# Performance work log

Hardware: AMD Instinct MI355X
Metric: run time of the kernel (lower is better)

## Reference

```python
import jax, jax.numpy as jnp
import numpy as np

NUM_HEADS = 14
NUM_KV_HEADS = 2
HEAD_DIM = 64
HIDDEN = 896
ROPE_THETA = 1000000.0
NEG_INF = -1e9


def _rope_tables(seq_len, dtype=jnp.float32):
    inv_freq = 1.0 / (ROPE_THETA ** (jnp.arange(0, HEAD_DIM, 2, dtype=jnp.float32) / HEAD_DIM))
    t = jnp.arange(seq_len, dtype=jnp.float32)
    freqs = t[:, None] * inv_freq[None, :]          # [S, hd/2]
    emb = jnp.concatenate((freqs, freqs), axis=-1)  # [S, hd]
    return jnp.cos(emb).astype(dtype), jnp.sin(emb).astype(dtype)


def _rotate_half(x):
    x1, x2 = x[..., : x.shape[-1] // 2], x[..., x.shape[-1] // 2 :]
    return jnp.concatenate((-x2, x1), axis=-1)


def setup_inputs() -> dict:
    key = jax.random.key(0)
    ks = jax.random.split(key, 6)
    B, S = 2, 2048
    hidden_states = jax.random.normal(ks[0], (B, S, HIDDEN), dtype=jnp.float32)
    # additive causal mask [1, 1, S, S]
    causal = jnp.tril(jnp.ones((S, S), dtype=bool))
    attention_mask = jnp.where(causal, 0.0, NEG_INF).astype(jnp.float32)[None, None]
    sd = 1.0 / np.sqrt(HIDDEN)
    Wq = jax.random.normal(ks[1], (HIDDEN, NUM_HEADS * HEAD_DIM), dtype=jnp.float32) * sd
    bq = jnp.zeros((NUM_HEADS * HEAD_DIM,), dtype=jnp.float32)
    Wk = jax.random.normal(ks[2], (HIDDEN, NUM_KV_HEADS * HEAD_DIM), dtype=jnp.float32) * sd
    bk = jnp.zeros((NUM_KV_HEADS * HEAD_DIM,), dtype=jnp.float32)
    Wv = jax.random.normal(ks[3], (HIDDEN, NUM_KV_HEADS * HEAD_DIM), dtype=jnp.float32) * sd
    bv = jnp.zeros((NUM_KV_HEADS * HEAD_DIM,), dtype=jnp.float32)
    Wo = jax.random.normal(ks[4], (NUM_HEADS * HEAD_DIM, HIDDEN), dtype=jnp.float32) * sd
    return {
        'hidden_states': hidden_states, 'attention_mask': attention_mask,
        'Wq': Wq, 'bq': bq, 'Wk': Wk, 'bk': bk, 'Wv': Wv, 'bv': bv, 'Wo': Wo,
    }


def reference(hidden_states, attention_mask, Wq, bq, Wk, bk, Wv, bv, Wo):
    B, S, _ = hidden_states.shape
    n_groups = NUM_HEADS // NUM_KV_HEADS
    q = (hidden_states @ Wq + bq).reshape(B, S, NUM_HEADS, HEAD_DIM)
    k = (hidden_states @ Wk + bk).reshape(B, S, NUM_KV_HEADS, HEAD_DIM)
    v = (hidden_states @ Wv + bv).reshape(B, S, NUM_KV_HEADS, HEAD_DIM)

    cos, sin = _rope_tables(S, hidden_states.dtype)
    cos = cos[None, :, None, :]
    sin = sin[None, :, None, :]
    q = q * cos + _rotate_half(q) * sin
    k = k * cos + _rotate_half(k) * sin

    # GQA: repeat kv heads to match query heads
    k = jnp.repeat(k, n_groups, axis=2)  # [B, S, nH, hd]
    v = jnp.repeat(v, n_groups, axis=2)

    q = q.transpose(0, 2, 1, 3)  # [B, nH, S, hd]
    k = k.transpose(0, 2, 1, 3)
    v = v.transpose(0, 2, 1, 3)

    scores = jnp.einsum('bhqd,bhkd->bhqk', q, k) / jnp.sqrt(jnp.float32(HEAD_DIM)).astype(q.dtype)
    scores = scores + attention_mask
    attn = jax.nn.softmax(scores, axis=-1)
    out = jnp.einsum('bhqk,bhkd->bhqd', attn, v)        # [B, nH, S, hd]
    out = out.transpose(0, 2, 1, 3).reshape(B, S, -1)   # [B, S, nH*hd]
    return out @ Wo
```

## Files before the change

### kernel.cpp

```cpp
#include <hip/hip_runtime.h>
#include <hip/hip_bf16.h>
#include <math.h>

#define NH 14
#define NKV 2
#define HD 64
#define HID 896
#define SEQ 2048
#define BATCH 2
#define KT 28

typedef __attribute__((ext_vector_type(8))) short short8;
typedef __attribute__((ext_vector_type(4))) float f32x4;
typedef unsigned short ushort_t;

__device__ __forceinline__ unsigned short f2b(float f) {
    unsigned int u = __float_as_uint(f);
    unsigned int r = (u + 0x7fffu + ((u >> 16) & 1u)) >> 16;
    return (unsigned short)r;
}

__global__ __launch_bounds__(256) void xcast_kernel(
    const float* __restrict__ X, ushort_t* __restrict__ Xb)
{
    size_t i = ((size_t)blockIdx.x * 256 + threadIdx.x) * 8;
    float4 a = *(const float4*)(X + i);
    float4 b = *(const float4*)(X + i + 4);
    short8 o;
    o[0] = f2b(a.x); o[1] = f2b(a.y); o[2] = f2b(a.z); o[3] = f2b(a.w);
    o[4] = f2b(b.x); o[5] = f2b(b.y); o[6] = f2b(b.z); o[7] = f2b(b.w);
    *(short8*)(Xb + i) = o;
}

__global__ __launch_bounds__(256) void wtrans_kernel(
    const float* __restrict__ Wq, const float* __restrict__ Wk,
    const float* __restrict__ Wv, const float* __restrict__ Wo,
    ushort_t* __restrict__ WqkvT, ushort_t* __restrict__ WoT)
{
    __shared__ float tile[32][33];
    const int tx = threadIdx.x, ty = threadIdx.y;
    const int z = blockIdx.z;
    const float* src; ushort_t* dst; int N, rowoff;
    if      (z == 0) { src = Wq; dst = WqkvT; N = HID; rowoff = 0;    }
    else if (z == 1) { src = Wk; dst = WqkvT; N = 128; rowoff = 896;  }
    else if (z == 2) { src = Wv; dst = WqkvT; N = 128; rowoff = 1024; }
    else             { src = Wo; dst = WoT;   N = HID; rowoff = 0;    }
    const int k0 = blockIdx.x * 32;
    const int n0 = blockIdx.y * 32;
    if (n0 >= N) return;
    #pragma unroll
    for (int i = 0; i < 4; ++i)
        tile[ty * 4 + i][tx] = src[(size_t)(k0 + ty * 4 + i) * N + n0 + tx];
    __syncthreads();
    #pragma unroll
    for (int i = 0; i < 4; ++i)
        dst[(size_t)(rowoff + n0 + ty * 4 + i) * HID + k0 + tx]
            = f2b(tile[tx][ty * 4 + i]);
}

#define LDA 40
__global__ __launch_bounds__(256) void qkv_kernel(
    const ushort_t* __restrict__ Xb, const ushort_t* __restrict__ WqkvT,
    const float* __restrict__ bq, const float* __restrict__ bk,
    const float* __restrict__ bv,
    ushort_t* __restrict__ qbuf, ushort_t* __restrict__ kbuf,
    ushort_t* __restrict__ vbuf)
{
    __shared__ ushort_t Asb[2][128 * LDA];
    __shared__ ushort_t Bsb[2][64 * LDA];
    const int tid  = threadIdx.x;
    const int w    = tid >> 6;
    const int lane = tid & 63;
    const int quad = lane >> 4;
    const int l16  = lane & 15;
    const int m0 = blockIdx.x * 128;
    const int nt = blockIdx.y;
    const int nb = nt * 64;

    const int ar0 = tid >> 2;
    const int ac8 = tid & 3;
    const ushort_t* Ag0 = Xb + (size_t)(m0 + ar0) * HID + ac8 * 8;
    const ushort_t* Ag1 = Xb + (size_t)(m0 + ar0 + 64) * HID + ac8 * 8;
    const ushort_t* Bg  = WqkvT + (size_t)(nb + ar0) * HID + ac8 * 8;

    f32x4 acc[2][4];
    #pragma unroll
    for (int mf = 0; mf < 2; ++mf)
        #pragma unroll
        for (int nf = 0; nf < 4; ++nf) acc[mf][nf] = (f32x4){0.f, 0.f, 0.f, 0.f};

    short8 aReg0, aReg1, bReg;
    aReg0 = *(const short8*)(Ag0);
    aReg1 = *(const short8*)(Ag1);
    bReg  = *(const short8*)(Bg);
    *(short8*)&Asb[0][ar0 * LDA + ac8 * 8]        = aReg0;
    *(short8*)&Asb[0][(ar0 + 64) * LDA + ac8 * 8] = aReg1;
    *(short8*)&Bsb[0][ar0 * LDA + ac8 * 8]        = bReg;
    aReg0 = *(const short8*)(Ag0 + 32);
    aReg1 = *(const short8*)(Ag1 + 32);
    bReg  = *(const short8*)(Bg  + 32);

    for (int ks = 0; ks < KT; ++ks) {
        __syncthreads();
        const int cur = ks & 1;
        if (ks + 1 < KT) {
            *(short8*)&Asb[cur ^ 1][ar0 * LDA + ac8 * 8]        = aReg0;
            *(short8*)&Asb[cur ^ 1][(ar0 + 64) * LDA + ac8 * 8] = aReg1;
            *(short8*)&Bsb[cur ^ 1][ar0 * LDA + ac8 * 8]        = bReg;
        }
        if (ks + 2 < KT) {
            aReg0 = *(const short8*)(Ag0 + (ks + 2) * 32);
            aReg1 = *(const short8*)(Ag1 + (ks + 2) * 32);
            bReg  = *(const short8*)(Bg  + (ks + 2) * 32);
        }
        const ushort_t* Ab = &Asb[cur][(w * 32 + l16) * LDA + quad * 8];
        short8 a0 = *(const short8*)Ab;
        short8 a1 = *(const short8*)(Ab + 16 * LDA);
        #pragma unroll
        for (int nf = 0; nf < 4; ++nf) {
            short8 bf = *(const short8*)&Bsb[cur][(nf * 16 + l16) * LDA + quad * 8];
            acc[0][nf] = __builtin_amdgcn_mfma_f32_16x16x32_bf16(a0, bf, acc[0][nf], 0, 0, 0);
            acc[1][nf] = __builtin_amdgcn_mfma_f32_16x16x32_bf16(a1, bf, acc[1][nf], 0, 0, 0);
        }
    }

    float bcol[4];
    #pragma unroll
    for (int f = 0; f < 4; ++f) {
        int d = f * 16 + l16;
        bcol[f] = (nt < 14) ? bq[nt * 64 + d]
                : (nt < 16) ? bk[(nt - 14) * 64 + d]
                            : bv[(nt - 16) * 64 + d];
    }
    const float lnth = 13.815510558f;
    float if0 = expf(-((float)l16)        / 32.0f * lnth);
    float if1 = expf(-((float)(l16 + 16)) / 32.0f * lnth);

    #pragma unroll
    for (int mf = 0; mf < 2; ++mf)
        #pragma unroll
        for (int r = 0; r < 4; ++r) {
            int grow = m0 + w * 32 + mf * 16 + quad * 4 + r;
            int b = grow >> 11;
            int s = grow & 2047;
            float v0 = acc[mf][0][r] + bcol[0];
            float v1 = acc[mf][1][r] + bcol[1];
            float v2 = acc[mf][2][r] + bcol[2];
            float v3 = acc[mf][3][r] + bcol[3];
            if (nt < 16) {
                float s0, c0, s1, c1;
                sincosf((float)s * if0, &s0, &c0);
                sincosf((float)s * if1, &s1, &c1);
                float n0 = v0 * c0 - v2 * s0;
                float n2 = v2 * c0 + v0 * s0;
                float n1 = v1 * c1 - v3 * s1;
                float n3 = v3 * c1 + v1 * s1;
                v0 = n0; v1 = n1; v2 = n2; v3 = n3;
            }
            if (nt < 14) {
                ushort_t* dst = qbuf + ((size_t)(b * NH + nt) * SEQ + s) * HD;
                dst[l16]      = f2b(v0);
                dst[l16 + 16] = f2b(v1);
                dst[l16 + 32] = f2b(v2);
                dst[l16 + 48] = f2b(v3);
            } else if (nt < 16) {
                ushort_t* dst = kbuf + ((size_t)(b * NKV + nt - 14) * SEQ + s) * HD;
                dst[l16]      = f2b(v0);
                dst[l16 + 16] = f2b(v1);
                dst[l16 + 32] = f2b(v2);
                dst[l16 + 48] = f2b(v3);
            } else {
                ushort_t* dst = vbuf + (size_t)(b * NKV + nt - 16) * HD * SEQ + s;
                dst[(size_t)(l16)      * SEQ] = f2b(v0);
                dst[(size_t)(l16 + 16) * SEQ] = f2b(v1);
                dst[(size_t)(l16 + 32) * SEQ] = f2b(v2);
                dst[(size_t)(l16 + 48) * SEQ] = f2b(v3);
            }
        }
}

#define LDP 76
__global__ __launch_bounds__(256) void attn_kernel(
    const ushort_t* __restrict__ qbuf, const ushort_t* __restrict__ kbuf,
    const ushort_t* __restrict__ vbuf, ushort_t* __restrict__ abuf)
{
    __shared__ ushort_t Ks[64 * LDP];
    __shared__ ushort_t Vt[64 * LDP];
    __shared__ ushort_t Ps[4][16 * LDP];

    const int tid  = threadIdx.x;
    const int w    = tid >> 6;
    const int lane = tid & 63;
    const int quad = lane >> 4;
    const int l16  = lane & 15;
    const int bi = blockIdx.x;
    const int h  = blockIdx.y;
    const int b  = blockIdx.z;
    const int kvh = h / (NH / NKV);

    const ushort_t* kb_h = kbuf + (size_t)(b * NKV + kvh) * SEQ * HD;
    const ushort_t* vt_h = vbuf + (size_t)(b * NKV + kvh) * HD * SEQ;

    for (int pass = 0; pass < 2; ++pass) {
        const int qt = pass ? (31 - bi) : bi;

        const ushort_t* qrow =
            qbuf + ((size_t)((b * NH + h) * SEQ) + qt * 64 + w * 16 + l16) * HD;
        short8 qf0 = *(const short8*)(qrow + quad * 8);
        short8 qf1 = *(const short8*)(qrow + 32 + quad * 8);

        f32x4 O[4];
        float m_i[4], l_i[4];
        #pragma unroll
        for (int n = 0; n < 4; ++n) O[n] = (f32x4){0.f, 0.f, 0.f, 0.f};
        #pragma unroll
        for (int r = 0; r < 4; ++r) { m_i[r] = -1e30f; l_i[r] = 0.0f; }

        for (int kt = 0; kt <= qt; ++kt) {
            __syncthreads();
            for (int i = tid; i < 512; i += 256) {
                int row = i >> 3, c8 = i & 7;
                *(short8*)&Ks[row * LDP + c8 * 8] =
                    *(const short8*)(kb_h + ((size_t)(kt * 64 + row)) * HD + c8 * 8);
                *(short8*)&Vt[row * LDP + c8 * 8] =
                    *(const short8*)(vt_h + (size_t)row * SEQ + kt * 64 + c8 * 8);
            }
            __syncthreads();

            f32x4 S[4];
            #pragma unroll
            for (int f = 0; f < 4; ++f) {
                S[f] = (f32x4){0.f, 0.f, 0.f, 0.f};
                short8 kf0 = *(const short8*)&Ks[(f * 16 + l16) * LDP + quad * 8];
                short8 kf1 = *(const short8*)&Ks[(f * 16 + l16) * LDP + 32 + quad * 8];
                S[f] = __builtin_amdgcn_mfma_f32_16x16x32_bf16(qf0, kf0, S[f], 0, 0, 0);
                S[f] = __builtin_amdgcn_mfma_f32_16x16x32_bf16(qf1, kf1, S[f], 0, 0, 0);
            }

            const bool diag = (kt == qt);
            float sc[4][4];
            #pragma unroll
            for (int f = 0; f < 4; ++f)
                #pragma unroll
                for (int r = 0; r < 4; ++r) {
                    float v = S[f][r] * 0.125f;
                    if (diag && (f * 16 + l16) > (w * 16 + quad * 4 + r)) v = -1e30f;
                    sc[f][r] = v;
                }

            float pm[4];
            #pragma unroll
            for (int r = 0; r < 4; ++r)
                pm[r] = fmaxf(fmaxf(sc[0][r], sc[1][r]), fmaxf(sc[2][r], sc[3][r]));
            #pragma unroll
            for (int off = 1; off < 16; off <<= 1)
                #pragma unroll
                for (int r = 0; r < 4; ++r)
                    pm[r] = fmaxf(pm[r], __shfl_xor(pm[r], off));

            float alpha[4], psum[4];
            #pragma unroll
            for (int r = 0; r < 4; ++r) {
                float mnew = fmaxf(m_i[r], pm[r]);
                alpha[r] = __expf(m_i[r] - mnew);
                m_i[r] = mnew;
                psum[r] = 0.0f;
            }
            #pragma unroll
            for (int f = 0; f < 4; ++f)
                #pragma unroll
                for (int r = 0; r < 4; ++r) {
                    float p = __expf(sc[f][r] - m_i[r]);
                    sc[f][r] = p;
                    psum[r] += p;
                }
            #pragma unroll
            for (int off = 1; off < 16; off <<= 1)
                #pragma unroll
                for (int r = 0; r < 4; ++r)
                    psum[r] += __shfl_xor(psum[r], off);
            #pragma unroll
            for (int r = 0; r < 4; ++r)
                l_i[r] = l_i[r] * alpha[r] + psum[r];
            #pragma unroll
            for (int n = 0; n < 4; ++n)
                #pragma unroll
                for (int r = 0; r < 4; ++r)
                    O[n][r] *= alpha[r];

            #pragma unroll
            for (int f = 0; f < 4; ++f)
                #pragma unroll
                for (int r = 0; r < 4; ++r)
                    Ps[w][(quad * 4 + r) * LDP + f * 16 + l16] = f2b(sc[f][r]);
            short8 pa0 = *(const short8*)&Ps[w][l16 * LDP + quad * 8];
            short8 pa1 = *(const short8*)&Ps[w][l16 * LDP + 32 + quad * 8];

            #pragma unroll
            for (int n = 0; n < 4; ++n) {
                short8 vf0 = *(const short8*)&Vt[(n * 16 + l16) * LDP + quad * 8];
                short8 vf1 = *(const short8*)&Vt[(n * 16 + l16) * LDP + 32 + quad * 8];
                O[n] = __builtin_amdgcn_mfma_f32_16x16x32_bf16(pa0, vf0, O[n], 0, 0, 0);
                O[n] = __builtin_amdgcn_mfma_f32_16x16x32_bf16(pa1, vf1, O[n], 0, 0, 0);
            }
        }

        float inv[4];
        #pragma unroll
        for (int r = 0; r < 4; ++r) inv[r] = 1.0f / l_i[r];
        #pragma unroll
        for (int n = 0; n < 4; ++n)
            #pragma unroll
            for (int r = 0; r < 4; ++r) {
                int rowg = qt * 64 + w * 16 + quad * 4 + r;
                abuf[(size_t)(b * SEQ + rowg) * HID + h * HD + n * 16 + l16]
                    = f2b(O[n][r] * inv[r]);
            }
    }
}

__global__ __launch_bounds__(256) void oproj_kernel(
    const ushort_t* __restrict__ A, const ushort_t* __restrict__ WoT,
    float* __restrict__ out)
{
    __shared__ ushort_t Asb[2][128 * LDA];
    __shared__ ushort_t Bsb[2][64 * LDA];
    const int tid  = threadIdx.x;
    const int w    = tid >> 6;
    const int lane = tid & 63;
    const int quad = lane >> 4;
    const int l16  = lane & 15;
    const int m0 = blockIdx.x * 128;
    const int n0 = blockIdx.y * 64;

    const int ar0 = tid >> 2;
    const int ac8 = tid & 3;
    const ushort_t* Ag0 = A + (size_t)(m0 + ar0) * HID + ac8 * 8;
    const ushort_t* Ag1 = A + (size_t)(m0 + ar0 + 64) * HID + ac8 * 8;
    const ushort_t* Bg  = WoT + (size_t)(n0 + ar0) * HID + ac8 * 8;

    f32x4 acc[2][4];
    #pragma unroll
    for (int mf = 0; mf < 2; ++mf)
        #pragma unroll
        for (int nf = 0; nf < 4; ++nf) acc[mf][nf] = (f32x4){0.f, 0.f, 0.f, 0.f};

    short8 aReg0, aReg1, bReg;
    aReg0 = *(const short8*)(Ag0);
    aReg1 = *(const short8*)(Ag1);
    bReg  = *(const short8*)(Bg);
    *(short8*)&Asb[0][ar0 * LDA + ac8 * 8]        = aReg0;
    *(short8*)&Asb[0][(ar0 + 64) * LDA + ac8 * 8] = aReg1;
    *(short8*)&Bsb[0][ar0 * LDA + ac8 * 8]        = bReg;
    aReg0 = *(const short8*)(Ag0 + 32);
    aReg1 = *(const short8*)(Ag1 + 32);
    bReg  = *(const short8*)(Bg  + 32);

    for (int ks = 0; ks < KT; ++ks) {
        __syncthreads();
        const int cur = ks & 1;
        if (ks + 1 < KT) {
            *(short8*)&Asb[cur ^ 1][ar0 * LDA + ac8 * 8]        = aReg0;
            *(short8*)&Asb[cur ^ 1][(ar0 + 64) * LDA + ac8 * 8] = aReg1;
            *(short8*)&Bsb[cur ^ 1][ar0 * LDA + ac8 * 8]        = bReg;
        }
        if (ks + 2 < KT) {
            aReg0 = *(const short8*)(Ag0 + (ks + 2) * 32);
            aReg1 = *(const short8*)(Ag1 + (ks + 2) * 32);
            bReg  = *(const short8*)(Bg  + (ks + 2) * 32);
        }
        const ushort_t* Ab = &Asb[cur][(w * 32 + l16) * LDA + quad * 8];
        short8 a0 = *(const short8*)Ab;
        short8 a1 = *(const short8*)(Ab + 16 * LDA);
        #pragma unroll
        for (int nf = 0; nf < 4; ++nf) {
            short8 bf = *(const short8*)&Bsb[cur][(nf * 16 + l16) * LDA + quad * 8];
            acc[0][nf] = __builtin_amdgcn_mfma_f32_16x16x32_bf16(a0, bf, acc[0][nf], 0, 0, 0);
            acc[1][nf] = __builtin_amdgcn_mfma_f32_16x16x32_bf16(a1, bf, acc[1][nf], 0, 0, 0);
        }
    }

    #pragma unroll
    for (int mf = 0; mf < 2; ++mf)
        #pragma unroll
        for (int r = 0; r < 4; ++r) {
            size_t rbase = (size_t)(m0 + w * 32 + mf * 16 + quad * 4 + r) * HID + n0;
            #pragma unroll
            for (int f = 0; f < 4; ++f)
                out[rbase + f * 16 + l16] = acc[mf][f][r];
        }
}

extern "C" void kernel_launch(void* const* d_in, const int* in_sizes, int n_in,
                              void* d_out, int out_size, void* d_ws, size_t ws_size,
                              hipStream_t stream) {
    const float* X  = (const float*)d_in[0];
    const float* Wq = (const float*)d_in[2];
    const float* bq = (const float*)d_in[3];
    const float* Wk = (const float*)d_in[4];
    const float* bk = (const float*)d_in[5];
    const float* Wv = (const float*)d_in[6];
    const float* bv = (const float*)d_in[7];
    const float* Wo = (const float*)d_in[8];
    float* out = (float*)d_out;

    ushort_t* ws    = (ushort_t*)d_ws;
    ushort_t* Xb    = ws;
    ushort_t* WqkvT = Xb    + 3670016;
    ushort_t* WoT   = WqkvT + 1032192;
    ushort_t* qbuf  = WoT   + 802816;
    ushort_t* kbuf  = qbuf  + 3670016;
    ushort_t* vbuf  = kbuf  + 524288;
    ushort_t* abufb = vbuf  + 524288;

    xcast_kernel<<<dim3(1792), 256, 0, stream>>>(X, Xb);
    wtrans_kernel<<<dim3(28, 28, 4), dim3(32, 8), 0, stream>>>(
        Wq, Wk, Wv, Wo, WqkvT, WoT);
    qkv_kernel<<<dim3(32, 18), 256, 0, stream>>>(
        Xb, WqkvT, bq, bk, bv, qbuf, kbuf, vbuf);
    attn_kernel<<<dim3(16, NH, BATCH), 256, 0, stream>>>(
        qbuf, kbuf, vbuf, abufb);
    oproj_kernel<<<dim3(32, 14), 256, 0, stream>>>(
        abufb, WoT, out);
}
```

Before: 207.7 us.

## Double-buffer K/V tiles, one query tile per block, fp16 PV path

The attention kernel now launches one block per query tile (32 blocks per head, heaviest first) instead of pairing light and heavy tiles in one block. K/V tiles are double-buffered in shared memory, with the next tile prefetched into registers, so each iteration needs one barrier instead of two. The softmax scale is folded into Q at projection time. V and P are stored in fp16 and use the f16 MFMA for better mantissa precision. The added LDS use and per-block Q load overhead could lower occupancy.

```diff
diff --git a/kernel.cpp b/kernel.cpp
--- a/kernel.cpp
+++ b/kernel.cpp
@@ -11,6 +11,7 @@
 #define KT 28
 
 typedef __attribute__((ext_vector_type(8))) short short8;
+typedef __attribute__((ext_vector_type(8))) _Float16 half8;
 typedef __attribute__((ext_vector_type(4))) float f32x4;
 typedef unsigned short ushort_t;
 
@@ -64,7 +65,7 @@
     const float* __restrict__ bq, const float* __restrict__ bk,
     const float* __restrict__ bv,
     ushort_t* __restrict__ qbuf, ushort_t* __restrict__ kbuf,
-    ushort_t* __restrict__ vbuf)
+    _Float16* __restrict__ vbuf)
 {
     __shared__ ushort_t Asb[2][128 * LDA];
     __shared__ ushort_t Bsb[2][64 * LDA];
@@ -159,10 +160,10 @@
             }
             if (nt < 14) {
                 ushort_t* dst = qbuf + ((size_t)(b * NH + nt) * SEQ + s) * HD;
-                dst[l16]      = f2b(v0);
-                dst[l16 + 16] = f2b(v1);
-                dst[l16 + 32] = f2b(v2);
-                dst[l16 + 48] = f2b(v3);
+                dst[l16]      = f2b(v0 * 0.125f);
+                dst[l16 + 16] = f2b(v1 * 0.125f);
+                dst[l16 + 32] = f2b(v2 * 0.125f);
+                dst[l16 + 48] = f2b(v3 * 0.125f);
             } else if (nt < 16) {
                 ushort_t* dst = kbuf + ((size_t)(b * NKV + nt - 14) * SEQ + s) * HD;
                 dst[l16]      = f2b(v0);
@@ -170,153 +171,173 @@
                 dst[l16 + 32] = f2b(v2);
                 dst[l16 + 48] = f2b(v3);
             } else {
-                ushort_t* dst = vbuf + (size_t)(b * NKV + nt - 16) * HD * SEQ + s;
-                dst[(size_t)(l16)      * SEQ] = f2b(v0);
-                dst[(size_t)(l16 + 16) * SEQ] = f2b(v1);
-                dst[(size_t)(l16 + 32) * SEQ] = f2b(v2);
-                dst[(size_t)(l16 + 48) * SEQ] = f2b(v3);
+                _Float16* dst = vbuf + (size_t)(b * NKV + nt - 16) * HD * SEQ + s;
+                dst[(size_t)(l16)      * SEQ] = (_Float16)v0;
+                dst[(size_t)(l16 + 16) * SEQ] = (_Float16)v1;
+                dst[(size_t)(l16 + 32) * SEQ] = (_Float16)v2;
+                dst[(size_t)(l16 + 48) * SEQ] = (_Float16)v3;
             }
         }
 }
 
-#define LDP 76
+#define LDP  76
+#define LDPS 72
 __global__ __launch_bounds__(256) void attn_kernel(
     const ushort_t* __restrict__ qbuf, const ushort_t* __restrict__ kbuf,
-    const ushort_t* __restrict__ vbuf, ushort_t* __restrict__ abuf)
+    const _Float16* __restrict__ vbuf, ushort_t* __restrict__ abuf)
 {
-    __shared__ ushort_t Ks[64 * LDP];
-    __shared__ ushort_t Vt[64 * LDP];
-    __shared__ ushort_t Ps[4][16 * LDP];
+    __shared__ ushort_t Ks[2][64 * LDP];
+    __shared__ _Float16 Vt[2][64 * LDP];
+    __shared__ _Float16 Ps[4][16 * LDPS];
 
     const int tid  = threadIdx.x;
     const int w    = tid >> 6;
     const int lane = tid & 63;
     const int quad = lane >> 4;
     const int l16  = lane & 15;
-    const int bi = blockIdx.x;
+    const int qt = 31 - blockIdx.x;
     const int h  = blockIdx.y;
     const int b  = blockIdx.z;
     const int kvh = h / (NH / NKV);
 
     const ushort_t* kb_h = kbuf + (size_t)(b * NKV + kvh) * SEQ * HD;
-    const ushort_t* vt_h = vbuf + (size_t)(b * NKV + kvh) * HD * SEQ;
-
-    for (int pass = 0; pass < 2; ++pass) {
-        const int qt = pass ? (31 - bi) : bi;
-
-        const ushort_t* qrow =
-            qbuf + ((size_t)((b * NH + h) * SEQ) + qt * 64 + w * 16 + l16) * HD;
-        short8 qf0 = *(const short8*)(qrow + quad * 8);
-        short8 qf1 = *(const short8*)(qrow + 32 + quad * 8);
-
-        f32x4 O[4];
-        float m_i[4], l_i[4];
-        #pragma unroll
-        for (int n = 0; n < 4; ++n) O[n] = (f32x4){0.f, 0.f, 0.f, 0.f};
-        #pragma unroll
-        for (int r = 0; r < 4; ++r) { m_i[r] = -1e30f; l_i[r] = 0.0f; }
-
-        for (int kt = 0; kt <= qt; ++kt) {
-            __syncthreads();
-            for (int i = tid; i < 512; i += 256) {
-                int row = i >> 3, c8 = i & 7;
-                *(short8*)&Ks[row * LDP + c8 * 8] =
-                    *(const short8*)(kb_h + ((size_t)(kt * 64 + row)) * HD + c8 * 8);
-                *(short8*)&Vt[row * LDP + c8 * 8] =
-                    *(const short8*)(vt_h + (size_t)row * SEQ + kt * 64 + c8 * 8);
+    const _Float16* vt_h = vbuf + (size_t)(b * NKV + kvh) * HD * SEQ;
+
+    const int sr0 = tid >> 3;
+    const int sc8 = tid & 7;
+
+    const ushort_t* qrow =
+        qbuf + ((size_t)((b * NH + h) * SEQ) + qt * 64 + w * 16 + l16) * HD;
+    short8 qf0 = *(const short8*)(qrow + quad * 8);
+    short8 qf1 = *(const short8*)(qrow + 32 + quad * 8);
+
+    f32x4 O[4];
+    float m_i[4], l_i[4];
+    #pragma unroll
+    for (int n = 0; n < 4; ++n) O[n] = (f32x4){0.f, 0.f, 0.f, 0.f};
+    #pragma unroll
+    for (int r = 0; r < 4; ++r) { m_i[r] = -1e30f; l_i[r] = 0.0f; }
+
+    short8 kr[2], vr[2];
+    #pragma unroll
+    for (int j = 0; j < 2; ++j) {
+        int row = sr0 + j * 32;
+        kr[j] = *(const short8*)(kb_h + (size_t)row * HD + sc8 * 8);
+        vr[j] = *(const short8*)(vt_h + (size_t)row * SEQ + sc8 * 8);
+    }
+
+    for (int kt = 0; kt <= qt; ++kt) {
+        const int cur = kt & 1;
+        #pragma unroll
+        for (int j = 0; j < 2; ++j) {
+            int row = sr0 + j * 32;
+            *(short8*)&Ks[cur][row * LDP + sc8 * 8] = kr[j];
+            *(short8*)&Vt[cur][row * LDP + sc8 * 8] = vr[j];
+        }
+        if (kt < qt) {
+            #pragma unroll
+            for (int j = 0; j < 2; ++j) {
+                int row = sr0 + j * 32;
+                kr[j] = *(const short8*)(kb_h + (size_t)((kt + 1) * 64 + row) * HD + sc8 * 8);
+                vr[j] = *(const short8*)(vt_h + (size_t)row * SEQ + (kt + 1) * 64 + sc8 * 8);
             }
-            __syncthreads();
-
-            f32x4 S[4];
-            #pragma unroll
-            for (int f = 0; f < 4; ++f) {
-                S[f] = (f32x4){0.f, 0.f, 0.f, 0.f};
-                short8 kf0 = *(const short8*)&Ks[(f * 16 + l16) * LDP + quad * 8];
-                short8 kf1 = *(const short8*)&Ks[(f * 16 + l16) * LDP + 32 + quad * 8];
-                S[f] = __builtin_amdgcn_mfma_f32_16x16x32_bf16(qf0, kf0, S[f], 0, 0, 0);
-                S[f] = __builtin_amdgcn_mfma_f32_16x16x32_bf16(qf1, kf1, S[f], 0, 0, 0);
-            }
-
-            const bool diag = (kt == qt);
-            float sc[4][4];
-            #pragma unroll
-            for (int f = 0; f < 4; ++f)
-                #pragma unroll
-                for (int r = 0; r < 4; ++r) {
-                    float v = S[f][r] * 0.125f;
-                    if (diag && (f * 16 + l16) > (w * 16 + quad * 4 + r)) v = -1e30f;
-                    sc[f][r] = v;
-                }
-
-            float pm[4];
-            #pragma unroll
-            for (int r = 0; r < 4; ++r)
-                pm[r] = fmaxf(fmaxf(sc[0][r], sc[1][r]), fmaxf(sc[2][r], sc[3][r]));
-            #pragma unroll
-            for (int off = 1; off < 16; off <<= 1)
-                #pragma unroll
-                for (int r = 0; r < 4; ++r)
-                    pm[r] = fmaxf(pm[r], __shfl_xor(pm[r], off));
-
-            float alpha[4], psum[4];
-            #pragma unroll
-            for (int r = 0; r < 4; ++r) {
-                float mnew = fmaxf(m_i[r], pm[r]);
-                alpha[r] = __expf(m_i[r] - mnew);
-                m_i[r] = mnew;
-                psum[r] = 0.0f;
-            }
-            #pragma unroll
-            for (int f = 0; f < 4; ++f)
-                #pragma unroll
-                for (int r = 0; r < 4; ++r) {
-                    float p = __expf(sc[f][r] - m_i[r]);
-                    sc[f][r] = p;
-                    psum[r] += p;
-                }
-            #pragma unroll
-            for (int off = 1; off < 16; off <<= 1)
-                #pragma unroll
-                for (int r = 0; r < 4; ++r)
-                    psum[r] += __shfl_xor(psum[r], off);
-            #pragma unroll
-            for (int r = 0; r < 4; ++r)
-                l_i[r] = l_i[r] * alpha[r] + psum[r];
-            #pragma unroll
-            for (int n = 0; n < 4; ++n)
-                #pragma unroll
-                for (int r = 0; r < 4; ++r)
-                    O[n][r] *= alpha[r];
-
+        }
+        __syncthreads();
+
+        f32x4 S[4];
+        #pragma unroll
+        for (int f = 0; f < 4; ++f) {
+            S[f] = (f32x4){0.f, 0.f, 0.f, 0.f};
+            short8 kf0 = *(const short8*)&Ks[cur][(f * 16 + l16) * LDP + quad * 8];
+            short8 kf1 = *(const short8*)&Ks[cur][(f * 16 + l16) * LDP + 32 + quad * 8];
+            S[f] = __builtin_amdgcn_mfma_f32_16x16x32_bf16(qf0, kf0, S[f], 0, 0, 0);
+            S[f] = __builtin_amdgcn_mfma_f32_16x16x32_bf16(qf1, kf1, S[f], 0, 0, 0);
+        }
+
+        const bool diag = (kt == qt);
+        float sc[4][4];
+        if (diag) {
             #pragma unroll
             for (int f = 0; f < 4; ++f)
                 #pragma unroll
                 for (int r = 0; r < 4; ++r)
-                    Ps[w][(quad * 4 + r) * LDP + f * 16 + l16] = f2b(sc[f][r]);
-            short8 pa0 = *(const short8*)&Ps[w][l16 * LDP + quad * 8];
-            short8 pa1 = *(const short8*)&Ps[w][l16 * LDP + 32 + quad * 8];
-
-            #pragma unroll
-            for (int n = 0; n < 4; ++n) {
-                short8 vf0 = *(const short8*)&Vt[(n * 16 + l16) * LDP + quad * 8];
-                short8 vf1 = *(const short8*)&Vt[(n * 16 + l16) * LDP + 32 + quad * 8];
-                O[n] = __builtin_amdgcn_mfma_f32_16x16x32_bf16(pa0, vf0, O[n], 0, 0, 0);
-                O[n] = __builtin_amdgcn_mfma_f32_16x16x32_bf16(pa1, vf1, O[n], 0, 0, 0);
+                    sc[f][r] = ((f * 16 + l16) > (w * 16 + quad * 4 + r))
+                             ? -1e30f : S[f][r];
+        } else {
+            #pragma unroll
+            for (int f = 0; f < 4; ++f)
+                #pragma unroll
+                for (int r = 0; r < 4; ++r) sc[f][r] = S[f][r];
+        }
+
+        float pm[4];
+        #pragma unroll
+        for (int r = 0; r < 4; ++r)
+            pm[r] = fmaxf(fmaxf(sc[0][r], sc[1][r]), fmaxf(sc[2][r], sc[3][r]));
+        #pragma unroll
+        for (int off = 1; off < 16; off <<= 1)
+            #pragma unroll
+            for (int r = 0; r < 4; ++r)
+                pm[r] = fmaxf(pm[r], __shfl_xor(pm[r], off));
+
+        float alpha[4], psum[4];
+        #pragma unroll
+        for (int r = 0; r < 4; ++r) {
+            float mnew = fmaxf(m_i[r], pm[r]);
+            alpha[r] = __expf(m_i[r] - mnew);
+            m_i[r] = mnew;
+            psum[r] = 0.0f;
+        }
+        #pragma unroll
+        for (int f = 0; f < 4; ++f)
+            #pragma unroll
+            for (int r = 0; r < 4; ++r) {
+                float p = __expf(sc[f][r] - m_i[r]);
+                sc[f][r] = p;
+                psum[r] += p;
             }
-        }
-
-        float inv[4];
-        #pragma unroll
-        for (int r = 0; r < 4; ++r) inv[r] = 1.0f / l_i[r];
+        #pragma unroll
+        for (int off = 1; off < 16; off <<= 1)
+            #pragma unroll
+            for (int r = 0; r < 4; ++r)
+                psum[r] += __shfl_xor(psum[r], off);
+        #pragma unroll
+        for (int r = 0; r < 4; ++r)
+            l_i[r] = l_i[r] * alpha[r] + psum[r];
         #pragma unroll
         for (int n = 0; n < 4; ++n)
             #pragma unroll
-            for (int r = 0; r < 4; ++r) {
-                int rowg = qt * 64 + w * 16 + quad * 4 + r;
-                abuf[(size_t)(b * SEQ + rowg) * HID + h * HD + n * 16 + l16]
-                    = f2b(O[n][r] * inv[r]);
-            }
+            for (int r = 0; r < 4; ++r)
+                O[n][r] *= alpha[r];
+
+        #pragma unroll
+        for (int f = 0; f < 4; ++f)
+            #pragma unroll
+            for (int r = 0; r < 4; ++r)
+                Ps[w][(quad * 4 + r) * LDPS + f * 16 + l16] = (_Float16)sc[f][r];
+        half8 pa0 = *(const half8*)&Ps[w][l16 * LDPS + quad * 8];
+        half8 pa1 = *(const half8*)&Ps[w][l16 * LDPS + 32 + quad * 8];
+
+        #pragma unroll
+        for (int n = 0; n < 4; ++n) {
+            half8 vf0 = *(const half8*)&Vt[cur][(n * 16 + l16) * LDP + quad * 8];
+            half8 vf1 = *(const half8*)&Vt[cur][(n * 16 + l16) * LDP + 32 + quad * 8];
+            O[n] = __builtin_amdgcn_mfma_f32_16x16x32_f16(pa0, vf0, O[n], 0, 0, 0);
+            O[n] = __builtin_amdgcn_mfma_f32_16x16x32_f16(pa1, vf1, O[n], 0, 0, 0);
+        }
     }
+
+    float inv[4];
+    #pragma unroll
+    for (int r = 0; r < 4; ++r) inv[r] = 1.0f / l_i[r];
+    #pragma unroll
+    for (int n = 0; n < 4; ++n)
+        #pragma unroll
+        for (int r = 0; r < 4; ++r) {
+            int rowg = qt * 64 + w * 16 + quad * 4 + r;
+            abuf[(size_t)(b * SEQ + rowg) * HID + h * HD + n * 16 + l16]
+                = f2b(O[n][r] * inv[r]);
+        }
 }
 
 __global__ __launch_bounds__(256) void oproj_kernel(
@@ -410,15 +431,15 @@
     ushort_t* WoT   = WqkvT + 1032192;
     ushort_t* qbuf  = WoT   + 802816;
     ushort_t* kbuf  = qbuf  + 3670016;
-    ushort_t* vbuf  = kbuf  + 524288;
-    ushort_t* abufb = vbuf  + 524288;
+    _Float16* vbuf  = (_Float16*)(kbuf + 524288);
+    ushort_t* abufb = (ushort_t*)(vbuf + 524288);
 
     xcast_kernel<<<dim3(1792), 256, 0, stream>>>(X, Xb);
     wtrans_kernel<<<dim3(28, 28, 4), dim3(32, 8), 0, stream>>>(
         Wq, Wk, Wv, Wo, WqkvT, WoT);
     qkv_kernel<<<dim3(32, 18), 256, 0, stream>>>(
         Xb, WqkvT, bq, bk, bv, qbuf, kbuf, vbuf);
-    attn_kernel<<<dim3(16, NH, BATCH), 256, 0, stream>>>(
+    attn_kernel<<<dim3(32, NH, BATCH), 256, 0, stream>>>(
         qbuf, kbuf, vbuf, abufb);
     oproj_kernel<<<dim3(32, 14), 256, 0, stream>>>(
         abufb, WoT, out);
```

After: 246.8 us. 1.19x slower.

## Split long causal attention rows across two blocks with a combine kernel

Applied to the files above, without the earlier changes.

Replaces the paired-query-tile scheme (one block handles tile bi and 31-bi) with a split-KV scheme on 48 blocks per head. Query tiles 16..31 are split into two KV chunks whose partial O, m and l are written to fp32 workspace, and a new combine kernel merges them. The goal is to raise block count and parallelism so the 256-CU GPU is better occupied (448 blocks before, 1344 now). The cost is extra global traffic for the partials and an extra kernel launch.

```diff
diff --git a/kernel.cpp b/kernel.cpp
--- a/kernel.cpp
+++ b/kernel.cpp
@@ -182,7 +182,8 @@
 #define LDP 76
 __global__ __launch_bounds__(256) void attn_kernel(
     const ushort_t* __restrict__ qbuf, const ushort_t* __restrict__ kbuf,
-    const ushort_t* __restrict__ vbuf, ushort_t* __restrict__ abuf)
+    const ushort_t* __restrict__ vbuf, ushort_t* __restrict__ abuf,
+    float* __restrict__ Opart, float* __restrict__ mlbuf)
 {
     __shared__ ushort_t Ks[64 * LDP];
     __shared__ ushort_t Vt[64 * LDP];
@@ -193,118 +194,123 @@
     const int lane = tid & 63;
     const int quad = lane >> 4;
     const int l16  = lane & 15;
-    const int bi = blockIdx.x;
+    const int bx = blockIdx.x;
     const int h  = blockIdx.y;
     const int b  = blockIdx.z;
     const int kvh = h / (NH / NKV);
 
+    int qt, t0, t1;
+    if (bx < 16)      { qt = 16 + bx;  t0 = 0;  t1 = 16;     }
+    else if (bx < 32) { qt = 47 - bx;  t0 = 16; t1 = qt + 1; }
+    else              { qt = 47 - bx;  t0 = 0;  t1 = qt + 1; }
+    const bool partial = (qt >= 16);
+    const int ch = (t0 == 16) ? 1 : 0;
+
     const ushort_t* kb_h = kbuf + (size_t)(b * NKV + kvh) * SEQ * HD;
     const ushort_t* vt_h = vbuf + (size_t)(b * NKV + kvh) * HD * SEQ;
 
-    for (int pass = 0; pass < 2; ++pass) {
-        const int qt = pass ? (31 - bi) : bi;
-
-        const ushort_t* qrow =
-            qbuf + ((size_t)((b * NH + h) * SEQ) + qt * 64 + w * 16 + l16) * HD;
-        short8 qf0 = *(const short8*)(qrow + quad * 8);
-        short8 qf1 = *(const short8*)(qrow + 32 + quad * 8);
-
-        f32x4 O[4];
-        float m_i[4], l_i[4];
-        #pragma unroll
-        for (int n = 0; n < 4; ++n) O[n] = (f32x4){0.f, 0.f, 0.f, 0.f};
-        #pragma unroll
-        for (int r = 0; r < 4; ++r) { m_i[r] = -1e30f; l_i[r] = 0.0f; }
-
-        for (int kt = 0; kt <= qt; ++kt) {
-            __syncthreads();
-            for (int i = tid; i < 512; i += 256) {
-                int row = i >> 3, c8 = i & 7;
-                *(short8*)&Ks[row * LDP + c8 * 8] =
-                    *(const short8*)(kb_h + ((size_t)(kt * 64 + row)) * HD + c8 * 8);
-                *(short8*)&Vt[row * LDP + c8 * 8] =
-                    *(const short8*)(vt_h + (size_t)row * SEQ + kt * 64 + c8 * 8);
-            }
-            __syncthreads();
-
-            f32x4 S[4];
-            #pragma unroll
-            for (int f = 0; f < 4; ++f) {
-                S[f] = (f32x4){0.f, 0.f, 0.f, 0.f};
-                short8 kf0 = *(const short8*)&Ks[(f * 16 + l16) * LDP + quad * 8];
-                short8 kf1 = *(const short8*)&Ks[(f * 16 + l16) * LDP + 32 + quad * 8];
-                S[f] = __builtin_amdgcn_mfma_f32_16x16x32_bf16(qf0, kf0, S[f], 0, 0, 0);
-                S[f] = __builtin_amdgcn_mfma_f32_16x16x32_bf16(qf1, kf1, S[f], 0, 0, 0);
-            }
-
-            const bool diag = (kt == qt);
-            float sc[4][4];
-            #pragma unroll
-            for (int f = 0; f < 4; ++f)
-                #pragma unroll
-                for (int r = 0; r < 4; ++r) {
-                    float v = S[f][r] * 0.125f;
-                    if (diag && (f * 16 + l16) > (w * 16 + quad * 4 + r)) v = -1e30f;
-                    sc[f][r] = v;
-                }
-
-            float pm[4];
+    const ushort_t* qrow =
+        qbuf + ((size_t)((b * NH + h) * SEQ) + qt * 64 + w * 16 + l16) * HD;
+    short8 qf0 = *(const short8*)(qrow + quad * 8);
+    short8 qf1 = *(const short8*)(qrow + 32 + quad * 8);
+
+    f32x4 O[4];
+    float m_i[4], l_i[4];
+    #pragma unroll
+    for (int n = 0; n < 4; ++n) O[n] = (f32x4){0.f, 0.f, 0.f, 0.f};
+    #pragma unroll
+    for (int r = 0; r < 4; ++r) { m_i[r] = -1e30f; l_i[r] = 0.0f; }
+
+    for (int kt = t0; kt < t1; ++kt) {
+        __syncthreads();
+        for (int i = tid; i < 512; i += 256) {
+            int row = i >> 3, c8 = i & 7;
+            *(short8*)&Ks[row * LDP + c8 * 8] =
+                *(const short8*)(kb_h + ((size_t)(kt * 64 + row)) * HD + c8 * 8);
+            *(short8*)&Vt[row * LDP + c8 * 8] =
+                *(const short8*)(vt_h + (size_t)row * SEQ + kt * 64 + c8 * 8);
+        }
+        __syncthreads();
+
+        f32x4 S[4];
+        #pragma unroll
+        for (int f = 0; f < 4; ++f) {
+            S[f] = (f32x4){0.f, 0.f, 0.f, 0.f};
+            short8 kf0 = *(const short8*)&Ks[(f * 16 + l16) * LDP + quad * 8];
+            short8 kf1 = *(const short8*)&Ks[(f * 16 + l16) * LDP + 32 + quad * 8];
+            S[f] = __builtin_amdgcn_mfma_f32_16x16x32_bf16(qf0, kf0, S[f], 0, 0, 0);
+            S[f] = __builtin_amdgcn_mfma_f32_16x16x32_bf16(qf1, kf1, S[f], 0, 0, 0);
+        }
+
+        const bool diag = (kt == qt);
+        float sc[4][4];
+        #pragma unroll
+        for (int f = 0; f < 4; ++f)
+            #pragma unroll
+            for (int r = 0; r < 4; ++r) {
+                float v = S[f][r] * 0.125f;
+                if (diag && (f * 16 + l16) > (w * 16 + quad * 4 + r)) v = -1e30f;
+                sc[f][r] = v;
+            }
+
+        float pm[4];
+        #pragma unroll
+        for (int r = 0; r < 4; ++r)
+            pm[r] = fmaxf(fmaxf(sc[0][r], sc[1][r]), fmaxf(sc[2][r], sc[3][r]));
+        #pragma unroll
+        for (int off = 1; off < 16; off <<= 1)
             #pragma unroll
             for (int r = 0; r < 4; ++r)
-                pm[r] = fmaxf(fmaxf(sc[0][r], sc[1][r]), fmaxf(sc[2][r], sc[3][r]));
-            #pragma unroll
-            for (int off = 1; off < 16; off <<= 1)
-                #pragma unroll
-                for (int r = 0; r < 4; ++r)
-                    pm[r] = fmaxf(pm[r], __shfl_xor(pm[r], off));
-
-            float alpha[4], psum[4];
+                pm[r] = fmaxf(pm[r], __shfl_xor(pm[r], off));
+
+        float alpha[4], psum[4];
+        #pragma unroll
+        for (int r = 0; r < 4; ++r) {
+            float mnew = fmaxf(m_i[r], pm[r]);
+            alpha[r] = __expf(m_i[r] - mnew);
+            m_i[r] = mnew;
+            psum[r] = 0.0f;
+        }
+        #pragma unroll
+        for (int f = 0; f < 4; ++f)
             #pragma unroll
             for (int r = 0; r < 4; ++r) {
-                float mnew = fmaxf(m_i[r], pm[r]);
-                alpha[r] = __expf(m_i[r] - mnew);
-                m_i[r] = mnew;
-                psum[r] = 0.0f;
-            }
-            #pragma unroll
-            for (int f = 0; f < 4; ++f)
-                #pragma unroll
-                for (int r = 0; r < 4; ++r) {
-                    float p = __expf(sc[f][r] - m_i[r]);
-                    sc[f][r] = p;
-                    psum[r] += p;
-                }
-            #pragma unroll
-            for (int off = 1; off < 16; off <<= 1)
-                #pragma unroll
-                for (int r = 0; r < 4; ++r)
-                    psum[r] += __shfl_xor(psum[r], off);
+                float p = __expf(sc[f][r] - m_i[r]);
+                sc[f][r] = p;
+                psum[r] += p;
+            }
+        #pragma unroll
+        for (int off = 1; off < 16; off <<= 1)
             #pragma unroll
             for (int r = 0; r < 4; ++r)
-                l_i[r] = l_i[r] * alpha[r] + psum[r];
-            #pragma unroll
-            for (int n = 0; n < 4; ++n)
-                #pragma unroll
-                for (int r = 0; r < 4; ++r)
-                    O[n][r] *= alpha[r];
-
-            #pragma unroll
-            for (int f = 0; f < 4; ++f)
-                #pragma unroll
-                for (int r = 0; r < 4; ++r)
-                    Ps[w][(quad * 4 + r) * LDP + f * 16 + l16] = f2b(sc[f][r]);
-            short8 pa0 = *(const short8*)&Ps[w][l16 * LDP + quad * 8];
-            short8 pa1 = *(const short8*)&Ps[w][l16 * LDP + 32 + quad * 8];
-
-            #pragma unroll
-            for (int n = 0; n < 4; ++n) {
-                short8 vf0 = *(const short8*)&Vt[(n * 16 + l16) * LDP + quad * 8];
-                short8 vf1 = *(const short8*)&Vt[(n * 16 + l16) * LDP + 32 + quad * 8];
-                O[n] = __builtin_amdgcn_mfma_f32_16x16x32_bf16(pa0, vf0, O[n], 0, 0, 0);
-                O[n] = __builtin_amdgcn_mfma_f32_16x16x32_bf16(pa1, vf1, O[n], 0, 0, 0);
-            }
-        }
-
+                psum[r] += __shfl_xor(psum[r], off);
+        #pragma unroll
+        for (int r = 0; r < 4; ++r)
+            l_i[r] = l_i[r] * alpha[r] + psum[r];
+        #pragma unroll
+        for (int n = 0; n < 4; ++n)
+            #pragma unroll
+            for (int r = 0; r < 4; ++r)
+                O[n][r] *= alpha[r];
+
+        #pragma unroll
+        for (int f = 0; f < 4; ++f)
+            #pragma unroll
+            for (int r = 0; r < 4; ++r)
+                Ps[w][(quad * 4 + r) * LDP + f * 16 + l16] = f2b(sc[f][r]);
+        short8 pa0 = *(const short8*)&Ps[w][l16 * LDP + quad * 8];
+        short8 pa1 = *(const short8*)&Ps[w][l16 * LDP + 32 + quad * 8];
+
+        #pragma unroll
+        for (int n = 0; n < 4; ++n) {
+            short8 vf0 = *(const short8*)&Vt[(n * 16 + l16) * LDP + quad * 8];
+            short8 vf1 = *(const short8*)&Vt[(n * 16 + l16) * LDP + 32 + quad * 8];
+            O[n] = __builtin_amdgcn_mfma_f32_16x16x32_bf16(pa0, vf0, O[n], 0, 0, 0);
+            O[n] = __builtin_amdgcn_mfma_f32_16x16x32_bf16(pa1, vf1, O[n], 0, 0, 0);
+        }
+    }
+
+    if (!partial) {
         float inv[4];
         #pragma unroll
         for (int r = 0; r < 4; ++r) inv[r] = 1.0f / l_i[r];
@@ -316,6 +322,58 @@
                 abuf[(size_t)(b * SEQ + rowg) * HID + h * HD + n * 16 + l16]
                     = f2b(O[n][r] * inv[r]);
             }
+    } else {
+        const size_t p = (((size_t)(b * NH + h) * 16 + (qt - 16)) * 2 + ch);
+        float* Od = Opart + p * 4096;
+        #pragma unroll
+        for (int n = 0; n < 4; ++n)
+            #pragma unroll
+            for (int r = 0; r < 4; ++r)
+                Od[(w * 16 + quad * 4 + r) * 64 + n * 16 + l16] = O[n][r];
+        if (l16 == 0) {
+            #pragma unroll
+            for (int r = 0; r < 4; ++r) {
+                size_t mi = (p * 64 + w * 16 + quad * 4 + r) * 2;
+                mlbuf[mi]     = m_i[r];
+                mlbuf[mi + 1] = l_i[r];
+            }
+        }
+    }
+}
+
+__global__ __launch_bounds__(256) void combine_kernel(
+    const float* __restrict__ Opart, const float* __restrict__ mlbuf,
+    ushort_t* __restrict__ abuf)
+{
+    const int tid = threadIdx.x;
+    const int row = tid >> 2;
+    const int qr  = tid & 3;
+    const int qt16 = blockIdx.x;
+    const int h = blockIdx.y;
+    const int b = blockIdx.z;
+
+    const size_t p0 = ((size_t)(b * NH + h) * 16 + qt16) * 2;
+    const float* ml0 = mlbuf + (p0 * 64 + row) * 2;
+    const float* ml1 = mlbuf + ((p0 + 1) * 64 + row) * 2;
+    float m0 = ml0[0], l0 = ml0[1];
+    float m1 = ml1[0], l1 = ml1[1];
+    float m = fmaxf(m0, m1);
+    float e0 = __expf(m0 - m), e1 = __expf(m1 - m);
+    float l = l0 * e0 + l1 * e1;
+    float inv = 1.0f / l;
+    float a0 = e0 * inv, a1 = e1 * inv;
+
+    const float4* O0 = (const float4*)(Opart + p0 * 4096 + row * 64 + qr * 16);
+    const float4* O1 = (const float4*)(Opart + (p0 + 1) * 4096 + row * 64 + qr * 16);
+    int rowg = (16 + qt16) * 64 + row;
+    ushort_t* op = abuf + (size_t)(b * SEQ + rowg) * HID + h * HD + qr * 16;
+    #pragma unroll
+    for (int g = 0; g < 4; ++g) {
+        float4 v0 = O0[g], v1 = O1[g];
+        op[g * 4 + 0] = f2b(v0.x * a0 + v1.x * a1);
+        op[g * 4 + 1] = f2b(v0.y * a0 + v1.y * a1);
+        op[g * 4 + 2] = f2b(v0.z * a0 + v1.z * a1);
+        op[g * 4 + 3] = f2b(v0.w * a0 + v1.w * a1);
     }
 }
 
@@ -412,14 +470,18 @@
     ushort_t* kbuf  = qbuf  + 3670016;
     ushort_t* vbuf  = kbuf  + 524288;
     ushort_t* abufb = vbuf  + 524288;
+    float*    Opart = (float*)(abufb + 3670016);
+    float*    mlbuf = Opart + 3670016;
 
     xcast_kernel<<<dim3(1792), 256, 0, stream>>>(X, Xb);
     wtrans_kernel<<<dim3(28, 28, 4), dim3(32, 8), 0, stream>>>(
         Wq, Wk, Wv, Wo, WqkvT, WoT);
     qkv_kernel<<<dim3(32, 18), 256, 0, stream>>>(
         Xb, WqkvT, bq, bk, bv, qbuf, kbuf, vbuf);
-    attn_kernel<<<dim3(16, NH, BATCH), 256, 0, stream>>>(
-        qbuf, kbuf, vbuf, abufb);
+    attn_kernel<<<dim3(48, NH, BATCH), 256, 0, stream>>>(
+        qbuf, kbuf, vbuf, abufb, Opart, mlbuf);
+    combine_kernel<<<dim3(16, NH, BATCH), 256, 0, stream>>>(
+        Opart, mlbuf, abufb);
     oproj_kernel<<<dim3(32, 14), 256, 0, stream>>>(
         abufb, WoT, out);
 }
```

Result: slower. 225.1 us (+8.4%).

## Compute transposed scores to keep P in registers and use fp16 PV MFMA

Applied to the files above, without the earlier changes.

The score MFMA now computes K·Q^T, so each lane holds one query row's probabilities. This removes the LDS round trip for P and collapses the softmax row reductions to two shuffles. P and V are stored as fp16 and fed to a 16x16x16 f16 MFMA straight from registers. The change also skips the masked upper-triangle blocks on the diagonal tile, folds the 1/sqrt(d) scale into Q at projection time, and vectorizes the output stores. The trade-offs are fp16 range and precision for V and P, and twice as many MFMA instructions for the PV product.

```diff
diff --git a/kernel.cpp b/kernel.cpp
--- a/kernel.cpp
+++ b/kernel.cpp
@@ -11,7 +11,9 @@
 #define KT 28
 
 typedef __attribute__((ext_vector_type(8))) short short8;
+typedef __attribute__((ext_vector_type(4))) short short4v;
 typedef __attribute__((ext_vector_type(4))) float f32x4;
+typedef __attribute__((ext_vector_type(4))) _Float16 half4;
 typedef unsigned short ushort_t;
 
 __device__ __forceinline__ unsigned short f2b(float f) {
@@ -64,7 +66,7 @@
     const float* __restrict__ bq, const float* __restrict__ bk,
     const float* __restrict__ bv,
     ushort_t* __restrict__ qbuf, ushort_t* __restrict__ kbuf,
-    ushort_t* __restrict__ vbuf)
+    _Float16* __restrict__ vbuf)
 {
     __shared__ ushort_t Asb[2][128 * LDA];
     __shared__ ushort_t Bsb[2][64 * LDA];
@@ -159,10 +161,10 @@
             }
             if (nt < 14) {
                 ushort_t* dst = qbuf + ((size_t)(b * NH + nt) * SEQ + s) * HD;
-                dst[l16]      = f2b(v0);
-                dst[l16 + 16] = f2b(v1);
-                dst[l16 + 32] = f2b(v2);
-                dst[l16 + 48] = f2b(v3);
+                dst[l16]      = f2b(v0 * 0.125f);
+                dst[l16 + 16] = f2b(v1 * 0.125f);
+                dst[l16 + 32] = f2b(v2 * 0.125f);
+                dst[l16 + 48] = f2b(v3 * 0.125f);
             } else if (nt < 16) {
                 ushort_t* dst = kbuf + ((size_t)(b * NKV + nt - 14) * SEQ + s) * HD;
                 dst[l16]      = f2b(v0);
@@ -170,11 +172,11 @@
                 dst[l16 + 32] = f2b(v2);
                 dst[l16 + 48] = f2b(v3);
             } else {
-                ushort_t* dst = vbuf + (size_t)(b * NKV + nt - 16) * HD * SEQ + s;
-                dst[(size_t)(l16)      * SEQ] = f2b(v0);
-                dst[(size_t)(l16 + 16) * SEQ] = f2b(v1);
-                dst[(size_t)(l16 + 32) * SEQ] = f2b(v2);
-                dst[(size_t)(l16 + 48) * SEQ] = f2b(v3);
+                _Float16* dst = vbuf + (size_t)(b * NKV + nt - 16) * HD * SEQ + s;
+                dst[(size_t)(l16)      * SEQ] = (_Float16)v0;
+                dst[(size_t)(l16 + 16) * SEQ] = (_Float16)v1;
+                dst[(size_t)(l16 + 32) * SEQ] = (_Float16)v2;
+                dst[(size_t)(l16 + 48) * SEQ] = (_Float16)v3;
             }
         }
 }
@@ -186,7 +188,6 @@
 {
     __shared__ ushort_t Ks[64 * LDP];
     __shared__ ushort_t Vt[64 * LDP];
-    __shared__ ushort_t Ps[4][16 * LDP];
 
     const int tid  = threadIdx.x;
     const int w    = tid >> 6;
@@ -210,11 +211,9 @@
         short8 qf1 = *(const short8*)(qrow + 32 + quad * 8);
 
         f32x4 O[4];
-        float m_i[4], l_i[4];
-        #pragma unroll
-        for (int n = 0; n < 4; ++n) O[n] = (f32x4){0.f, 0.f, 0.f, 0.f};
-        #pragma unroll
-        for (int r = 0; r < 4; ++r) { m_i[r] = -1e30f; l_i[r] = 0.0f; }
+        #pragma unroll
+        for (int mf = 0; mf < 4; ++mf) O[mf] = (f32x4){0.f, 0.f, 0.f, 0.f};
+        float m_i = -1e30f, l_i = 0.0f;
 
         for (int kt = 0; kt <= qt; ++kt) {
             __syncthreads();
@@ -227,95 +226,87 @@
             }
             __syncthreads();
 
+            const bool diag = (kt == qt);
+
             f32x4 S[4];
             #pragma unroll
             for (int f = 0; f < 4; ++f) {
                 S[f] = (f32x4){0.f, 0.f, 0.f, 0.f};
-                short8 kf0 = *(const short8*)&Ks[(f * 16 + l16) * LDP + quad * 8];
-                short8 kf1 = *(const short8*)&Ks[(f * 16 + l16) * LDP + 32 + quad * 8];
-                S[f] = __builtin_amdgcn_mfma_f32_16x16x32_bf16(qf0, kf0, S[f], 0, 0, 0);
-                S[f] = __builtin_amdgcn_mfma_f32_16x16x32_bf16(qf1, kf1, S[f], 0, 0, 0);
+                if (!diag || f <= w) {
+                    short8 kf0 = *(const short8*)&Ks[(f * 16 + l16) * LDP + quad * 8];
+                    short8 kf1 = *(const short8*)&Ks[(f * 16 + l16) * LDP + 32 + quad * 8];
+                    S[f] = __builtin_amdgcn_mfma_f32_16x16x32_bf16(kf0, qf0, S[f], 0, 0, 0);
+                    S[f] = __builtin_amdgcn_mfma_f32_16x16x32_bf16(kf1, qf1, S[f], 0, 0, 0);
+                }
             }
 
-            const bool diag = (kt == qt);
+            const int myrow = w * 16 + l16;
             float sc[4][4];
+            float cmax = -1e30f;
             #pragma unroll
             for (int f = 0; f < 4; ++f)
                 #pragma unroll
                 for (int r = 0; r < 4; ++r) {
-                    float v = S[f][r] * 0.125f;
-                    if (diag && (f * 16 + l16) > (w * 16 + quad * 4 + r)) v = -1e30f;
+                    float v = S[f][r];
+                    if (diag && (f * 16 + quad * 4 + r) > myrow) v = -1e30f;
                     sc[f][r] = v;
+                    cmax = fmaxf(cmax, v);
                 }
-
-            float pm[4];
-            #pragma unroll
-            for (int r = 0; r < 4; ++r)
-                pm[r] = fmaxf(fmaxf(sc[0][r], sc[1][r]), fmaxf(sc[2][r], sc[3][r]));
-            #pragma unroll
-            for (int off = 1; off < 16; off <<= 1)
-                #pragma unroll
-                for (int r = 0; r < 4; ++r)
-                    pm[r] = fmaxf(pm[r], __shfl_xor(pm[r], off));
-
-            float alpha[4], psum[4];
-            #pragma unroll
-            for (int r = 0; r < 4; ++r) {
-                float mnew = fmaxf(m_i[r], pm[r]);
-                alpha[r] = __expf(m_i[r] - mnew);
-                m_i[r] = mnew;
-                psum[r] = 0.0f;
-            }
+            cmax = fmaxf(cmax, __shfl_xor(cmax, 16));
+            cmax = fmaxf(cmax, __shfl_xor(cmax, 32));
+
+            float m_new = fmaxf(m_i, cmax);
+            float alpha = __expf(m_i - m_new);
+            m_i = m_new;
+
+            float psum = 0.0f;
             #pragma unroll
             for (int f = 0; f < 4; ++f)
                 #pragma unroll
                 for (int r = 0; r < 4; ++r) {
-                    float p = __expf(sc[f][r] - m_i[r]);
+                    float p = __expf(sc[f][r] - m_new);
                     sc[f][r] = p;
-                    psum[r] += p;
+                    psum += p;
                 }
-            #pragma unroll
-            for (int off = 1; off < 16; off <<= 1)
+            psum += __shfl_xor(psum, 16);
+            psum += __shfl_xor(psum, 32);
+            l_i = l_i * alpha + psum;
+
+            #pragma unroll
+            for (int mf = 0; mf < 4; ++mf)
                 #pragma unroll
                 for (int r = 0; r < 4; ++r)
-                    psum[r] += __shfl_xor(psum[r], off);
-            #pragma unroll
-            for (int r = 0; r < 4; ++r)
-                l_i[r] = l_i[r] * alpha[r] + psum[r];
-            #pragma unroll
-            for (int n = 0; n < 4; ++n)
-                #pragma unroll
-                for (int r = 0; r < 4; ++r)
-                    O[n][r] *= alpha[r];
-
+                    O[mf][r] *= alpha;
+
+            half4 pb[4];
             #pragma unroll
             for (int f = 0; f < 4; ++f)
                 #pragma unroll
-                for (int r = 0; r < 4; ++r)
-                    Ps[w][(quad * 4 + r) * LDP + f * 16 + l16] = f2b(sc[f][r]);
-            short8 pa0 = *(const short8*)&Ps[w][l16 * LDP + quad * 8];
-            short8 pa1 = *(const short8*)&Ps[w][l16 * LDP + 32 + quad * 8];
-
-            #pragma unroll
-            for (int n = 0; n < 4; ++n) {
-                short8 vf0 = *(const short8*)&Vt[(n * 16 + l16) * LDP + quad * 8];
-                short8 vf1 = *(const short8*)&Vt[(n * 16 + l16) * LDP + 32 + quad * 8];
-                O[n] = __builtin_amdgcn_mfma_f32_16x16x32_bf16(pa0, vf0, O[n], 0, 0, 0);
-                O[n] = __builtin_amdgcn_mfma_f32_16x16x32_bf16(pa1, vf1, O[n], 0, 0, 0);
+                for (int j = 0; j < 4; ++j)
+                    pb[f][j] = (_Float16)sc[f][j];
+
+            #pragma unroll
+            for (int mf = 0; mf < 4; ++mf) {
+                const ushort_t* vb = &Vt[(mf * 16 + l16) * LDP + quad * 4];
+                #pragma unroll
+                for (int kc = 0; kc < 4; ++kc) {
+                    if (!diag || kc <= w) {
+                        half4 va = *(const half4*)(vb + kc * 16);
+                        O[mf] = __builtin_amdgcn_mfma_f32_16x16x16f16(va, pb[kc], O[mf], 0, 0, 0);
+                    }
+                }
             }
         }
 
-        float inv[4];
-        #pragma unroll
-        for (int r = 0; r < 4; ++r) inv[r] = 1.0f / l_i[r];
-        #pragma unroll
-        for (int n = 0; n < 4; ++n)
-            #pragma unroll
-            for (int r = 0; r < 4; ++r) {
-                int rowg = qt * 64 + w * 16 + quad * 4 + r;
-                abuf[(size_t)(b * SEQ + rowg) * HID + h * HD + n * 16 + l16]
-                    = f2b(O[n][r] * inv[r]);
-            }
+        float inv = 1.0f / l_i;
+        ushort_t* op = abuf + (size_t)(b * SEQ + qt * 64 + w * 16 + l16) * HID + h * HD;
+        #pragma unroll
+        for (int mf = 0; mf < 4; ++mf) {
+            short4v st;
+            #pragma unroll
+            for (int r = 0; r < 4; ++r) st[r] = (short)f2b(O[mf][r] * inv);
+            *(short4v*)(op + mf * 16 + quad * 4) = st;
+        }
     }
 }
 
@@ -410,8 +401,8 @@
     ushort_t* WoT   = WqkvT + 1032192;
     ushort_t* qbuf  = WoT   + 802816;
     ushort_t* kbuf  = qbuf  + 3670016;
-    ushort_t* vbuf  = kbuf  + 524288;
-    ushort_t* abufb = vbuf  + 524288;
+    _Float16* vbuf  = (_Float16*)(kbuf + 524288);
+    ushort_t* abufb = (ushort_t*)(vbuf + 524288);
 
     xcast_kernel<<<dim3(1792), 256, 0, stream>>>(X, Xb);
     wtrans_kernel<<<dim3(28, 28, 4), dim3(32, 8), 0, stream>>>(
@@ -419,7 +410,7 @@
     qkv_kernel<<<dim3(32, 18), 256, 0, stream>>>(
         Xb, WqkvT, bq, bk, bv, qbuf, kbuf, vbuf);
     attn_kernel<<<dim3(16, NH, BATCH), 256, 0, stream>>>(
-        qbuf, kbuf, vbuf, abufb);
+        qbuf, kbuf, (const ushort_t*)vbuf, abufb);
     oproj_kernel<<<dim3(32, 14), 256, 0, stream>>>(
         abufb, WoT, out);
 }
```

Measured after the change: 207.9 us. No clear change (+0.1%).
